# Optimization experiments

Measured on AMD Instinct MI355X. Metric: run time of the kernel, lower is better.

The kernel has to match this reference:

```python
import jax, jax.numpy as jnp
import numpy as np

N_NODES = 100000
D = 128            # hidden_size*2
N_EDGES = 1600000  # avg degree 16
NUM_LABELS = 1024


def setup_inputs() -> dict:
    key = jax.random.key(0)
    ks = jax.random.split(key, 16)
    inputs = jax.random.normal(ks[0], (N_NODES, D), dtype=jnp.float32)
    src = jax.random.randint(ks[1], (N_EDGES,), 0, N_NODES, dtype=jnp.int64)
    dst = jax.random.randint(ks[2], (N_EDGES,), 0, N_NODES, dtype=jnp.int64)
    s = 0.05
    # GIN layer 1 (conv linear) + residual block 1
    eps1 = jnp.zeros((), dtype=jnp.float32)
    W1 = jax.random.normal(ks[3], (D, D), dtype=jnp.float32) * s
    b1 = jnp.zeros((D,), dtype=jnp.float32)
    rW1 = jax.random.normal(ks[4], (D, D), dtype=jnp.float32) * s
    rb1 = jnp.zeros((D,), dtype=jnp.float32)
    # GIN layer 2 + residual block 2
    eps2 = jnp.zeros((), dtype=jnp.float32)
    W2 = jax.random.normal(ks[5], (D, D), dtype=jnp.float32) * s
    b2 = jnp.zeros((D,), dtype=jnp.float32)
    rW2 = jax.random.normal(ks[6], (D, D), dtype=jnp.float32) * s
    rb2 = jnp.zeros((D,), dtype=jnp.float32)
    # final multi-label head
    linW = jax.random.normal(ks[7], (D, NUM_LABELS), dtype=jnp.float32) * s
    linb = jnp.zeros((NUM_LABELS,), dtype=jnp.float32)
    return dict(inputs=inputs, src=src, dst=dst,
                eps1=eps1, W1=W1, b1=b1, rW1=rW1, rb1=rb1,
                eps2=eps2, W2=W2, b2=b2, rW2=rW2, rb2=rb2,
                linW=linW, linb=linb)


def reference(inputs, src, dst, eps1, W1, b1, rW1, rb1,
              eps2, W2, b2, rW2, rb2, linW, linb):
    n = inputs.shape[0]

    def gin_conv(h, eps, W, b):
        # sum-aggregate neighbor features: irregular gather + scatter-add
        agg = jax.ops.segment_sum(h[src], dst, num_segments=n)  # [N, D]
        return ((1.0 + eps) * h + agg) @ W + b

    def residual_block(h, rW, rb):
        # Sequential(ReLU, Dropout(eval=identity), Residual(D, D))
        h = jax.nn.relu(h)
        return h + jax.nn.relu(h @ rW + rb)

    h1 = residual_block(gin_conv(inputs, eps1, W1, b1), rW1, rb1)
    h2 = residual_block(gin_conv(h1, eps2, W2, b2), rW2, rb2)

    stacked = jnp.stack([h1, h2], axis=1)   # [N, n_layers, D] == stack_embed
    pooled = stacked.mean(axis=1)           # [N, D]
    return pooled @ linW + linb             # [N, NUM_LABELS]
```

## Files before the change

### kernel.cpp

```cpp
#include <hip/hip_runtime.h>

#define DIM 128
#define NLAB 1024
#define MT 64
#define LDK 136

typedef __bf16 bf16x4 __attribute__((ext_vector_type(4)));
typedef __bf16 bf16x8 __attribute__((ext_vector_type(8)));
typedef float  f32x4  __attribute__((ext_vector_type(4)));

__global__ __launch_bounds__(256) void k_hist(
    const int* __restrict__ dst, int* __restrict__ cnt, int nE) {
  int e = blockIdx.x * 256 + threadIdx.x;
  if (e < nE) atomicAdd(&cnt[dst[e]], 1);
}

__global__ __launch_bounds__(1024) void k_scan(
    const int* __restrict__ cnt, int* __restrict__ off,
    int* __restrict__ cur, int n) {
  __shared__ int part[1024];
  const int t = threadIdx.x;
  const int per = (n + 1023) >> 10;
  const int start = t * per;
  const int end = min(start + per, n);
  int s = 0;
  for (int i = start; i < end; ++i) s += cnt[i];
  part[t] = s;
  __syncthreads();
  for (int d = 1; d < 1024; d <<= 1) {
    int v = (t >= d) ? part[t - d] : 0;
    __syncthreads();
    part[t] += v;
    __syncthreads();
  }
  int excl = (t == 0) ? 0 : part[t - 1];
  if (t == 1023) off[n] = part[1023];
  for (int i = start; i < end; ++i) {
    int c = cnt[i];
    off[i] = excl;
    cur[i] = excl;
    excl += c;
  }
}

__global__ __launch_bounds__(256) void k_binfill(
    const int* __restrict__ src, const int* __restrict__ dst,
    int* __restrict__ cur, int* __restrict__ eidx, int nE) {
  int e = blockIdx.x * 256 + threadIdx.x;
  if (e < nE) {
    int p = atomicAdd(&cur[dst[e]], 1);
    eidx[p] = src[e];
  }
}

__global__ __launch_bounds__(256) void k_gather(
    const float* __restrict__ h, const int* __restrict__ off,
    const int* __restrict__ eidx, float* __restrict__ agg, int n) {
  int node = blockIdx.x * 8 + (threadIdx.x >> 5);
  if (node >= n) return;
  int c = (threadIdx.x & 31) << 2;
  int beg = off[node], end = off[node + 1];
  float4 a0 = make_float4(0.f, 0.f, 0.f, 0.f);
  float4 a1 = a0, a2 = a0, a3 = a0;
  int e = beg;
  for (; e + 4 <= end; e += 4) {
    int s0 = eidx[e + 0];
    int s1 = eidx[e + 1];
    int s2 = eidx[e + 2];
    int s3 = eidx[e + 3];
    float4 v0 = *(const float4*)(h + (size_t)s0 * DIM + c);
    float4 v1 = *(const float4*)(h + (size_t)s1 * DIM + c);
    float4 v2 = *(const float4*)(h + (size_t)s2 * DIM + c);
    float4 v3 = *(const float4*)(h + (size_t)s3 * DIM + c);
    a0.x += v0.x; a0.y += v0.y; a0.z += v0.z; a0.w += v0.w;
    a1.x += v1.x; a1.y += v1.y; a1.z += v1.z; a1.w += v1.w;
    a2.x += v2.x; a2.y += v2.y; a2.z += v2.z; a2.w += v2.w;
    a3.x += v3.x; a3.y += v3.y; a3.z += v3.z; a3.w += v3.w;
  }
  for (; e < end; ++e) {
    int s = eidx[e];
    float4 v = *(const float4*)(h + (size_t)s * DIM + c);
    a0.x += v.x; a0.y += v.y; a0.z += v.z; a0.w += v.w;
  }
  a0.x += a1.x + a2.x + a3.x;
  a0.y += a1.y + a2.y + a3.y;
  a0.z += a1.z + a2.z + a3.z;
  a0.w += a1.w + a2.w + a3.w;
  *(float4*)(agg + (size_t)node * DIM + c) = a0;
}

__device__ __forceinline__ void conv_residual_tile(
    const float* __restrict__ hin, const float* __restrict__ agg, float e1,
    const float* __restrict__ W, const float* __restrict__ bias,
    const float* __restrict__ rW, const float* __restrict__ rbias,
    __bf16 (*As)[LDK], __bf16 (*Bs)[LDK],
    int rowBase, int n, int t, float ho[4][2][4]) {
#pragma unroll
  for (int it = 0; it < 8; ++it) {
    int idx = (it * 256 + t) << 2;
    int r = idx >> 7, c = idx & 127;
    int node = rowBase + r;
    float4 a4 = make_float4(0.f, 0.f, 0.f, 0.f);
    float4 g4 = a4;
    if (node < n) {
      a4 = *(const float4*)(hin + (size_t)node * DIM + c);
      g4 = *(const float4*)(agg + (size_t)node * DIM + c);
    }
    bf16x4 v;
    v[0] = (__bf16)(e1 * a4.x + g4.x);
    v[1] = (__bf16)(e1 * a4.y + g4.y);
    v[2] = (__bf16)(e1 * a4.z + g4.z);
    v[3] = (__bf16)(e1 * a4.w + g4.w);
    *(bf16x4*)&As[r][c] = v;
  }
  {
    int nloc = t & 127;
    int kh = (t >> 7) << 6;
#pragma unroll
    for (int kk = 0; kk < 64; ++kk) {
      int k = kh + kk;
      Bs[nloc][k] = (__bf16)W[(size_t)k * DIM + nloc];
    }
  }
  __syncthreads();

  const int wv = t >> 6, lane = t & 63;
  const int quad = lane >> 4, l16 = lane & 15;
  f32x4 acc[4][2];
#pragma unroll
  for (int i = 0; i < 4; ++i) {
    acc[i][0] = f32x4{0.f, 0.f, 0.f, 0.f};
    acc[i][1] = f32x4{0.f, 0.f, 0.f, 0.f};
  }
#pragma unroll
  for (int kc = 0; kc < 4; ++kc) {
    int kb = kc * 32 + quad * 8;
    bf16x8 b0 = *(const bf16x8*)&Bs[wv * 32 + l16][kb];
    bf16x8 b1 = *(const bf16x8*)&Bs[wv * 32 + 16 + l16][kb];
#pragma unroll
    for (int rt = 0; rt < 4; ++rt) {
      bf16x8 a = *(const bf16x8*)&As[rt * 16 + l16][kb];
      acc[rt][0] = __builtin_amdgcn_mfma_f32_16x16x32_bf16(a, b0, acc[rt][0], 0, 0, 0);
      acc[rt][1] = __builtin_amdgcn_mfma_f32_16x16x32_bf16(a, b1, acc[rt][1], 0, 0, 0);
    }
  }

  float hm[4][2][4];
#pragma unroll
  for (int rt = 0; rt < 4; ++rt)
#pragma unroll
    for (int ct = 0; ct < 2; ++ct) {
      float bv = bias[wv * 32 + ct * 16 + l16];
#pragma unroll
      for (int r = 0; r < 4; ++r)
        hm[rt][ct][r] = fmaxf(acc[rt][ct][r] + bv, 0.f);
    }

  __syncthreads();

#pragma unroll
  for (int rt = 0; rt < 4; ++rt)
#pragma unroll
    for (int ct = 0; ct < 2; ++ct) {
      int col = wv * 32 + ct * 16 + l16;
#pragma unroll
      for (int r = 0; r < 4; ++r)
        As[rt * 16 + quad * 4 + r][col] = (__bf16)hm[rt][ct][r];
    }
  {
    int nloc = t & 127;
    int kh = (t >> 7) << 6;
#pragma unroll
    for (int kk = 0; kk < 64; ++kk) {
      int k = kh + kk;
      Bs[nloc][k] = (__bf16)rW[(size_t)k * DIM + nloc];
    }
  }
  __syncthreads();

#pragma unroll
  for (int i = 0; i < 4; ++i) {
    acc[i][0] = f32x4{0.f, 0.f, 0.f, 0.f};
    acc[i][1] = f32x4{0.f, 0.f, 0.f, 0.f};
  }
#pragma unroll
  for (int kc = 0; kc < 4; ++kc) {
    int kb = kc * 32 + quad * 8;
    bf16x8 b0 = *(const bf16x8*)&Bs[wv * 32 + l16][kb];
    bf16x8 b1 = *(const bf16x8*)&Bs[wv * 32 + 16 + l16][kb];
#pragma unroll
    for (int rt = 0; rt < 4; ++rt) {
      bf16x8 a = *(const bf16x8*)&As[rt * 16 + l16][kb];
      acc[rt][0] = __builtin_amdgcn_mfma_f32_16x16x32_bf16(a, b0, acc[rt][0], 0, 0, 0);
      acc[rt][1] = __builtin_amdgcn_mfma_f32_16x16x32_bf16(a, b1, acc[rt][1], 0, 0, 0);
    }
  }

#pragma unroll
  for (int rt = 0; rt < 4; ++rt)
#pragma unroll
    for (int ct = 0; ct < 2; ++ct) {
      float bv = rbias[wv * 32 + ct * 16 + l16];
#pragma unroll
      for (int r = 0; r < 4; ++r)
        ho[rt][ct][r] = hm[rt][ct][r] + fmaxf(acc[rt][ct][r] + bv, 0.f);
    }
}

__global__ __launch_bounds__(256) void k_layer1(
    const float* __restrict__ hin, const float* __restrict__ agg,
    const float* __restrict__ epsp, const float* __restrict__ W,
    const float* __restrict__ bias, const float* __restrict__ rW,
    const float* __restrict__ rbias, float* __restrict__ h1, int n) {
  __shared__ __bf16 As[MT][LDK];
  __shared__ __bf16 Bs[DIM][LDK];
  const int t = threadIdx.x;
  const int rowBase = blockIdx.x * MT;
  float ho[4][2][4];
  conv_residual_tile(hin, agg, 1.0f + epsp[0], W, bias, rW, rbias,
                     As, Bs, rowBase, n, t, ho);
  const int wv = t >> 6, lane = t & 63;
  const int quad = lane >> 4, l16 = lane & 15;
#pragma unroll
  for (int rt = 0; rt < 4; ++rt)
#pragma unroll
    for (int ct = 0; ct < 2; ++ct) {
      int ncol = wv * 32 + ct * 16 + l16;
#pragma unroll
      for (int r = 0; r < 4; ++r) {
        int node = rowBase + rt * 16 + quad * 4 + r;
        if (node < n) h1[(size_t)node * DIM + ncol] = ho[rt][ct][r];
      }
    }
}

__global__ __launch_bounds__(256) void k_layer2(
    const float* __restrict__ h1, const float* __restrict__ agg,
    const float* __restrict__ epsp, const float* __restrict__ W,
    const float* __restrict__ bias, const float* __restrict__ rW,
    const float* __restrict__ rbias, __bf16* __restrict__ pooled, int n) {
  __shared__ __bf16 As[MT][LDK];
  __shared__ __bf16 Bs[DIM][LDK];
  const int t = threadIdx.x;
  const int rowBase = blockIdx.x * MT;
  float ho[4][2][4];
  conv_residual_tile(h1, agg, 1.0f + epsp[0], W, bias, rW, rbias,
                     As, Bs, rowBase, n, t, ho);
  const int wv = t >> 6, lane = t & 63;
  const int quad = lane >> 4, l16 = lane & 15;
#pragma unroll
  for (int rt = 0; rt < 4; ++rt)
#pragma unroll
    for (int ct = 0; ct < 2; ++ct) {
      int col = wv * 32 + ct * 16 + l16;
#pragma unroll
      for (int r = 0; r < 4; ++r) {
        int node = rowBase + rt * 16 + quad * 4 + r;
        if (node < n) {
          float h1v = h1[(size_t)node * DIM + col];
          pooled[(size_t)node * DIM + col] =
              (__bf16)(0.5f * (h1v + ho[rt][ct][r]));
        }
      }
    }
}

__global__ __launch_bounds__(256) void k_final_p(
    const __bf16* __restrict__ pooled, const float* __restrict__ W,
    const float* __restrict__ bias, float* __restrict__ out, int n) {
  __shared__ __bf16 As[MT][LDK];
  __shared__ __bf16 Bs[DIM][LDK];
  const int t = threadIdx.x;
  const int rowBase = blockIdx.x * MT;
  const int nb = blockIdx.y << 7;

#pragma unroll
  for (int it = 0; it < 4; ++it) {
    int idx = (it * 256 + t) << 3;
    int r = idx >> 7, c = idx & 127;
    int node = rowBase + r;
    bf16x8 v;
#pragma unroll
    for (int j = 0; j < 8; ++j) v[j] = (__bf16)0.f;
    if (node < n) v = *(const bf16x8*)(pooled + (size_t)node * DIM + c);
    *(bf16x8*)&As[r][c] = v;
  }
  {
    int nloc = t & 127;
    int kh = (t >> 7) << 6;
#pragma unroll
    for (int kk = 0; kk < 64; ++kk) {
      int k = kh + kk;
      Bs[nloc][k] = (__bf16)W[(size_t)k * NLAB + nb + nloc];
    }
  }
  __syncthreads();

  const int wv = t >> 6, lane = t & 63;
  const int quad = lane >> 4, l16 = lane & 15;
  f32x4 acc[4][2];
#pragma unroll
  for (int i = 0; i < 4; ++i) {
    acc[i][0] = f32x4{0.f, 0.f, 0.f, 0.f};
    acc[i][1] = f32x4{0.f, 0.f, 0.f, 0.f};
  }

#pragma unroll
  for (int kc = 0; kc < 4; ++kc) {
    int kb = kc * 32 + quad * 8;
    bf16x8 b0 = *(const bf16x8*)&Bs[wv * 32 + l16][kb];
    bf16x8 b1 = *(const bf16x8*)&Bs[wv * 32 + 16 + l16][kb];
#pragma unroll
    for (int rt = 0; rt < 4; ++rt) {
      bf16x8 a = *(const bf16x8*)&As[rt * 16 + l16][kb];
      acc[rt][0] = __builtin_amdgcn_mfma_f32_16x16x32_bf16(a, b0, acc[rt][0], 0, 0, 0);
      acc[rt][1] = __builtin_amdgcn_mfma_f32_16x16x32_bf16(a, b1, acc[rt][1], 0, 0, 0);
    }
  }

#pragma unroll
  for (int rt = 0; rt < 4; ++rt)
#pragma unroll
    for (int ct = 0; ct < 2; ++ct) {
      int ncol = wv * 32 + ct * 16 + l16;
      float bv = bias[nb + ncol];
#pragma unroll
      for (int r = 0; r < 4; ++r) {
        int node = rowBase + rt * 16 + quad * 4 + r;
        if (node < n)
          out[(size_t)node * NLAB + nb + ncol] = acc[rt][ct][r] + bv;
      }
    }
}

extern "C" void kernel_launch(void* const* d_in, const int* in_sizes, int n_in,
                              void* d_out, int out_size, void* d_ws, size_t ws_size,
                              hipStream_t stream) {
  const float* inputs = (const float*)d_in[0];
  const int*   src    = (const int*)d_in[1];
  const int*   dst    = (const int*)d_in[2];
  const float* eps1   = (const float*)d_in[3];
  const float* W1     = (const float*)d_in[4];
  const float* b1     = (const float*)d_in[5];
  const float* rW1    = (const float*)d_in[6];
  const float* rb1    = (const float*)d_in[7];
  const float* eps2   = (const float*)d_in[8];
  const float* W2     = (const float*)d_in[9];
  const float* b2     = (const float*)d_in[10];
  const float* rW2    = (const float*)d_in[11];
  const float* rb2    = (const float*)d_in[12];
  const float* linW   = (const float*)d_in[13];
  const float* linb   = (const float*)d_in[14];
  float* out = (float*)d_out;

  const int n = in_sizes[0] / DIM;
  const int E = in_sizes[1];
  const size_t bufB = (size_t)n * DIM * sizeof(float);

  float*  agg    = (float*)d_ws;
  float*  h1     = (float*)((char*)d_ws + bufB);
  __bf16* pooled = (__bf16*)((char*)d_ws + 2 * bufB);

  int* eidx = (int*)d_out;
  int* off  = eidx + E;
  int* cur  = off + (n + 1);

  const int rowBlocks = (n + MT - 1) / MT;
  const int eBlocks = (E + 255) / 256;
  const int gBlocks = (n + 7) / 8;
  dim3 fgrid(rowBlocks, NLAB / DIM);

  hipMemsetAsync(cur, 0, (size_t)n * sizeof(int), stream);
  k_hist<<<eBlocks, 256, 0, stream>>>(dst, cur, E);
  k_scan<<<1, 1024, 0, stream>>>(cur, off, cur, n);
  k_binfill<<<eBlocks, 256, 0, stream>>>(src, dst, cur, eidx, E);

  k_gather<<<gBlocks, 256, 0, stream>>>(inputs, off, eidx, agg, n);
  k_layer1<<<rowBlocks, 256, 0, stream>>>(inputs, agg, eps1, W1, b1, rW1, rb1, h1, n);
  k_gather<<<gBlocks, 256, 0, stream>>>(h1, off, eidx, agg, n);
  k_layer2<<<rowBlocks, 256, 0, stream>>>(h1, agg, eps2, W2, b2, rW2, rb2,
                                          pooled, n);
  k_final_p<<<fgrid, 256, 0, stream>>>(pooled, linW, linb, out, n);
}
```

Before: 1.313 ms.

## Store node features in bf16 and pre-transpose weights once for MFMA

```diff
diff --git a/kernel.cpp b/kernel.cpp
--- a/kernel.cpp
+++ b/kernel.cpp
@@ -53,227 +53,92 @@
   }
 }
 
-__global__ __launch_bounds__(256) void k_gather(
-    const float* __restrict__ h, const int* __restrict__ off,
+__global__ __launch_bounds__(256) void k_cvt_w(
+    const float* __restrict__ W1, const float* __restrict__ rW1,
+    const float* __restrict__ W2, const float* __restrict__ rW2,
+    const float* __restrict__ linW,
+    __bf16* __restrict__ W1b, __bf16* __restrict__ rW1b,
+    __bf16* __restrict__ W2b, __bf16* __restrict__ rW2b,
+    __bf16* __restrict__ linWb) {
+  int tid = blockIdx.x * 256 + threadIdx.x;
+  if (tid < 65536) {
+    int m = tid >> 14, i = tid & 16383;
+    int nn = i >> 7, k = i & 127;
+    const float* S = (m == 0) ? W1 : (m == 1) ? rW1 : (m == 2) ? W2 : rW2;
+    __bf16* D = (m == 0) ? W1b : (m == 1) ? rW1b : (m == 2) ? W2b : rW2b;
+    D[nn * DIM + k] = (__bf16)S[(size_t)k * DIM + nn];
+  } else if (tid < 196608) {
+    int i = tid - 65536;
+    int nn = i >> 7, k = i & 127;
+    linWb[(size_t)nn * DIM + k] = (__bf16)linW[(size_t)k * NLAB + nn];
+  }
+}
+
+__global__ __launch_bounds__(256) void k_cvt_in(
+    const float* __restrict__ x, __bf16* __restrict__ y, int n) {
+  size_t i = (size_t)blockIdx.x * 256 + threadIdx.x;
+  if (i >= (size_t)n * 16) return;
+  float4 a = ((const float4*)x)[i * 2];
+  float4 b = ((const float4*)x)[i * 2 + 1];
+  bf16x8 v;
+  v[0] = (__bf16)a.x; v[1] = (__bf16)a.y; v[2] = (__bf16)a.z; v[3] = (__bf16)a.w;
+  v[4] = (__bf16)b.x; v[5] = (__bf16)b.y; v[6] = (__bf16)b.z; v[7] = (__bf16)b.w;
+  ((bf16x8*)y)[i] = v;
+}
+
+__global__ __launch_bounds__(256) void k_gather_b(
+    const __bf16* __restrict__ h, const int* __restrict__ off,
     const int* __restrict__ eidx, float* __restrict__ agg, int n) {
-  int node = blockIdx.x * 8 + (threadIdx.x >> 5);
+  int node = blockIdx.x * 16 + (threadIdx.x >> 4);
   if (node >= n) return;
-  int c = (threadIdx.x & 31) << 2;
+  int c = (threadIdx.x & 15) << 3;
   int beg = off[node], end = off[node + 1];
-  float4 a0 = make_float4(0.f, 0.f, 0.f, 0.f);
-  float4 a1 = a0, a2 = a0, a3 = a0;
+  float a0[8] = {0.f, 0.f, 0.f, 0.f, 0.f, 0.f, 0.f, 0.f};
+  float a1[8] = {0.f, 0.f, 0.f, 0.f, 0.f, 0.f, 0.f, 0.f};
+  float a2[8] = {0.f, 0.f, 0.f, 0.f, 0.f, 0.f, 0.f, 0.f};
+  float a3[8] = {0.f, 0.f, 0.f, 0.f, 0.f, 0.f, 0.f, 0.f};
   int e = beg;
   for (; e + 4 <= end; e += 4) {
     int s0 = eidx[e + 0];
     int s1 = eidx[e + 1];
     int s2 = eidx[e + 2];
     int s3 = eidx[e + 3];
-    float4 v0 = *(const float4*)(h + (size_t)s0 * DIM + c);
-    float4 v1 = *(const float4*)(h + (size_t)s1 * DIM + c);
-    float4 v2 = *(const float4*)(h + (size_t)s2 * DIM + c);
-    float4 v3 = *(const float4*)(h + (size_t)s3 * DIM + c);
-    a0.x += v0.x; a0.y += v0.y; a0.z += v0.z; a0.w += v0.w;
-    a1.x += v1.x; a1.y += v1.y; a1.z += v1.z; a1.w += v1.w;
-    a2.x += v2.x; a2.y += v2.y; a2.z += v2.z; a2.w += v2.w;
-    a3.x += v3.x; a3.y += v3.y; a3.z += v3.z; a3.w += v3.w;
+    bf16x8 v0 = *(const bf16x8*)(h + (size_t)s0 * DIM + c);
+    bf16x8 v1 = *(const bf16x8*)(h + (size_t)s1 * DIM + c);
+    bf16x8 v2 = *(const bf16x8*)(h + (size_t)s2 * DIM + c);
+    bf16x8 v3 = *(const bf16x8*)(h + (size_t)s3 * DIM + c);
+#pragma unroll
+    for (int j = 0; j < 8; ++j) {
+      a0[j] += (float)v0[j];
+      a1[j] += (float)v1[j];
+      a2[j] += (float)v2[j];
+      a3[j] += (float)v3[j];
+    }
   }
   for (; e < end; ++e) {
     int s = eidx[e];
-    float4 v = *(const float4*)(h + (size_t)s * DIM + c);
-    a0.x += v.x; a0.y += v.y; a0.z += v.z; a0.w += v.w;
-  }
-  a0.x += a1.x + a2.x + a3.x;
-  a0.y += a1.y + a2.y + a3.y;
-  a0.z += a1.z + a2.z + a3.z;
-  a0.w += a1.w + a2.w + a3.w;
-  *(float4*)(agg + (size_t)node * DIM + c) = a0;
+    bf16x8 v = *(const bf16x8*)(h + (size_t)s * DIM + c);
+#pragma unroll
+    for (int j = 0; j < 8; ++j) a0[j] += (float)v[j];
+  }
+  float4 o0, o1;
+  o0.x = a0[0] + a1[0] + a2[0] + a3[0];
+  o0.y = a0[1] + a1[1] + a2[1] + a3[1];
+  o0.z = a0[2] + a1[2] + a2[2] + a3[2];
+  o0.w = a0[3] + a1[3] + a2[3] + a3[3];
+  o1.x = a0[4] + a1[4] + a2[4] + a3[4];
+  o1.y = a0[5] + a1[5] + a2[5] + a3[5];
+  o1.z = a0[6] + a1[6] + a2[6] + a3[6];
+  o1.w = a0[7] + a1[7] + a2[7] + a3[7];
+  *(float4*)(agg + (size_t)node * DIM + c) = o0;
+  *(float4*)(agg + (size_t)node * DIM + c + 4) = o1;
 }
 
 __device__ __forceinline__ void conv_residual_tile(
-    const float* __restrict__ hin, const float* __restrict__ agg, float e1,
-    const float* __restrict__ W, const float* __restrict__ bias,
-    const float* __restrict__ rW, const float* __restrict__ rbias,
-    __bf16 (*As)[LDK], __bf16 (*Bs)[LDK],
-    int rowBase, int n, int t, float ho[4][2][4]) {
-#pragma unroll
-  for (int it = 0; it < 8; ++it) {
-    int idx = (it * 256 + t) << 2;
-    int r = idx >> 7, c = idx & 127;
-    int node = rowBase + r;
-    float4 a4 = make_float4(0.f, 0.f, 0.f, 0.f);
-    float4 g4 = a4;
-    if (node < n) {
-      a4 = *(const float4*)(hin + (size_t)node * DIM + c);
-      g4 = *(const float4*)(agg + (size_t)node * DIM + c);
-    }
-    bf16x4 v;
-    v[0] = (__bf16)(e1 * a4.x + g4.x);
-    v[1] = (__bf16)(e1 * a4.y + g4.y);
-    v[2] = (__bf16)(e1 * a4.z + g4.z);
-    v[3] = (__bf16)(e1 * a4.w + g4.w);
-    *(bf16x4*)&As[r][c] = v;
-  }
-  {
-    int nloc = t & 127;
-    int kh = (t >> 7) << 6;
-#pragma unroll
-    for (int kk = 0; kk < 64; ++kk) {
-      int k = kh + kk;
-      Bs[nloc][k] = (__bf16)W[(size_t)k * DIM + nloc];
-    }
-  }
-  __syncthreads();
-
-  const int wv = t >> 6, lane = t & 63;
-  const int quad = lane >> 4, l16 = lane & 15;
-  f32x4 acc[4][2];
-#pragma unroll
-  for (int i = 0; i < 4; ++i) {
-    acc[i][0] = f32x4{0.f, 0.f, 0.f, 0.f};
-    acc[i][1] = f32x4{0.f, 0.f, 0.f, 0.f};
-  }
-#pragma unroll
-  for (int kc = 0; kc < 4; ++kc) {
-    int kb = kc * 32 + quad * 8;
-    bf16x8 b0 = *(const bf16x8*)&Bs[wv * 32 + l16][kb];
-    bf16x8 b1 = *(const bf16x8*)&Bs[wv * 32 + 16 + l16][kb];
-#pragma unroll
-    for (int rt = 0; rt < 4; ++rt) {
-      bf16x8 a = *(const bf16x8*)&As[rt * 16 + l16][kb];
-      acc[rt][0] = __builtin_amdgcn_mfma_f32_16x16x32_bf16(a, b0, acc[rt][0], 0, 0, 0);
-      acc[rt][1] = __builtin_amdgcn_mfma_f32_16x16x32_bf16(a, b1, acc[rt][1], 0, 0, 0);
-    }
-  }
-
-  float hm[4][2][4];
-#pragma unroll
-  for (int rt = 0; rt < 4; ++rt)
-#pragma unroll
-    for (int ct = 0; ct < 2; ++ct) {
-      float bv = bias[wv * 32 + ct * 16 + l16];
-#pragma unroll
-      for (int r = 0; r < 4; ++r)
-        hm[rt][ct][r] = fmaxf(acc[rt][ct][r] + bv, 0.f);
-    }
-
-  __syncthreads();
-
-#pragma unroll
-  for (int rt = 0; rt < 4; ++rt)
-#pragma unroll
-    for (int ct = 0; ct < 2; ++ct) {
-      int col = wv * 32 + ct * 16 + l16;
-#pragma unroll
-      for (int r = 0; r < 4; ++r)
-        As[rt * 16 + quad * 4 + r][col] = (__bf16)hm[rt][ct][r];
-    }
-  {
-    int nloc = t & 127;
-    int kh = (t >> 7) << 6;
-#pragma unroll
-    for (int kk = 0; kk < 64; ++kk) {
-      int k = kh + kk;
-      Bs[nloc][k] = (__bf16)rW[(size_t)k * DIM + nloc];
-    }
-  }
-  __syncthreads();
-
-#pragma unroll
-  for (int i = 0; i < 4; ++i) {
-    acc[i][0] = f32x4{0.f, 0.f, 0.f, 0.f};
-    acc[i][1] = f32x4{0.f, 0.f, 0.f, 0.f};
-  }
-#pragma unroll
-  for (int kc = 0; kc < 4; ++kc) {
-    int kb = kc * 32 + quad * 8;
-    bf16x8 b0 = *(const bf16x8*)&Bs[wv * 32 + l16][kb];
-    bf16x8 b1 = *(const bf16x8*)&Bs[wv * 32 + 16 + l16][kb];
-#pragma unroll
-    for (int rt = 0; rt < 4; ++rt) {
-      bf16x8 a = *(const bf16x8*)&As[rt * 16 + l16][kb];
-      acc[rt][0] = __builtin_amdgcn_mfma_f32_16x16x32_bf16(a, b0, acc[rt][0], 0, 0, 0);
-      acc[rt][1] = __builtin_amdgcn_mfma_f32_16x16x32_bf16(a, b1, acc[rt][1], 0, 0, 0);
-    }
-  }
-
-#pragma unroll
-  for (int rt = 0; rt < 4; ++rt)
-#pragma unroll
-    for (int ct = 0; ct < 2; ++ct) {
-      float bv = rbias[wv * 32 + ct * 16 + l16];
-#pragma unroll
-      for (int r = 0; r < 4; ++r)
-        ho[rt][ct][r] = hm[rt][ct][r] + fmaxf(acc[rt][ct][r] + bv, 0.f);
-    }
-}
-
-__global__ __launch_bounds__(256) void k_layer1(
-    const float* __restrict__ hin, const float* __restrict__ agg,
-    const float* __restrict__ epsp, const float* __restrict__ W,
-    const float* __restrict__ bias, const float* __restrict__ rW,
-    const float* __restrict__ rbias, float* __restrict__ h1, int n) {
-  __shared__ __bf16 As[MT][LDK];
-  __shared__ __bf16 Bs[DIM][LDK];
-  const int t = threadIdx.x;
-  const int rowBase = blockIdx.x * MT;
-  float ho[4][2][4];
-  conv_residual_tile(hin, agg, 1.0f + epsp[0], W, bias, rW, rbias,
-                     As, Bs, rowBase, n, t, ho);
-  const int wv = t >> 6, lane = t & 63;
-  const int quad = lane >> 4, l16 = lane & 15;
-#pragma unroll
-  for (int rt = 0; rt < 4; ++rt)
-#pragma unroll
-    for (int ct = 0; ct < 2; ++ct) {
-      int ncol = wv * 32 + ct * 16 + l16;
-#pragma unroll
-      for (int r = 0; r < 4; ++r) {
-        int node = rowBase + rt * 16 + quad * 4 + r;
-        if (node < n) h1[(size_t)node * DIM + ncol] = ho[rt][ct][r];
-      }
-    }
-}
-
-__global__ __launch_bounds__(256) void k_layer2(
-    const float* __restrict__ h1, const float* __restrict__ agg,
-    const float* __restrict__ epsp, const float* __restrict__ W,
-    const float* __restrict__ bias, const float* __restrict__ rW,
-    const float* __restrict__ rbias, __bf16* __restrict__ pooled, int n) {
-  __shared__ __bf16 As[MT][LDK];
-  __shared__ __bf16 Bs[DIM][LDK];
-  const int t = threadIdx.x;
-  const int rowBase = blockIdx.x * MT;
-  float ho[4][2][4];
-  conv_residual_tile(h1, agg, 1.0f + epsp[0], W, bias, rW, rbias,
-                     As, Bs, rowBase, n, t, ho);
-  const int wv = t >> 6, lane = t & 63;
-  const int quad = lane >> 4, l16 = lane & 15;
-#pragma unroll
-  for (int rt = 0; rt < 4; ++rt)
-#pragma unroll
-    for (int ct = 0; ct < 2; ++ct) {
-      int col = wv * 32 + ct * 16 + l16;
-#pragma unroll
-      for (int r = 0; r < 4; ++r) {
-        int node = rowBase + rt * 16 + quad * 4 + r;
-        if (node < n) {
-          float h1v = h1[(size_t)node * DIM + col];
-          pooled[(size_t)node * DIM + col] =
-              (__bf16)(0.5f * (h1v + ho[rt][ct][r]));
-        }
-      }
-    }
-}
-
-__global__ __launch_bounds__(256) void k_final_p(
-    const __bf16* __restrict__ pooled, const float* __restrict__ W,
-    const float* __restrict__ bias, float* __restrict__ out, int n) {
-  __shared__ __bf16 As[MT][LDK];
-  __shared__ __bf16 Bs[DIM][LDK];
-  const int t = threadIdx.x;
-  const int rowBase = blockIdx.x * MT;
-  const int nb = blockIdx.y << 7;
-
+    const __bf16* __restrict__ hinb, const float* __restrict__ agg, float e1,
+    const __bf16* __restrict__ Wb, const float* __restrict__ bias,
+    const __bf16* __restrict__ rWb, const float* __restrict__ rbias,
+    __bf16 (*As)[LDK], int rowBase, int n, int t, float ho[4][2][4]) {
 #pragma unroll
   for (int it = 0; it < 4; ++it) {
     int idx = (it * 256 + t) << 3;
@@ -282,34 +147,195 @@
     bf16x8 v;
 #pragma unroll
     for (int j = 0; j < 8; ++j) v[j] = (__bf16)0.f;
-    if (node < n) v = *(const bf16x8*)(pooled + (size_t)node * DIM + c);
+    if (node < n) {
+      bf16x8 hv = *(const bf16x8*)(hinb + (size_t)node * DIM + c);
+      float4 g0 = *(const float4*)(agg + (size_t)node * DIM + c);
+      float4 g1 = *(const float4*)(agg + (size_t)node * DIM + c + 4);
+      v[0] = (__bf16)(e1 * (float)hv[0] + g0.x);
+      v[1] = (__bf16)(e1 * (float)hv[1] + g0.y);
+      v[2] = (__bf16)(e1 * (float)hv[2] + g0.z);
+      v[3] = (__bf16)(e1 * (float)hv[3] + g0.w);
+      v[4] = (__bf16)(e1 * (float)hv[4] + g1.x);
+      v[5] = (__bf16)(e1 * (float)hv[5] + g1.y);
+      v[6] = (__bf16)(e1 * (float)hv[6] + g1.z);
+      v[7] = (__bf16)(e1 * (float)hv[7] + g1.w);
+    }
     *(bf16x8*)&As[r][c] = v;
-  }
-  {
-    int nloc = t & 127;
-    int kh = (t >> 7) << 6;
-#pragma unroll
-    for (int kk = 0; kk < 64; ++kk) {
-      int k = kh + kk;
-      Bs[nloc][k] = (__bf16)W[(size_t)k * NLAB + nb + nloc];
-    }
   }
   __syncthreads();
 
   const int wv = t >> 6, lane = t & 63;
   const int quad = lane >> 4, l16 = lane & 15;
+  const __bf16* B0p = Wb + (size_t)(wv * 32 + l16) * DIM;
+  const __bf16* B1p = Wb + (size_t)(wv * 32 + 16 + l16) * DIM;
+
   f32x4 acc[4][2];
 #pragma unroll
   for (int i = 0; i < 4; ++i) {
     acc[i][0] = f32x4{0.f, 0.f, 0.f, 0.f};
     acc[i][1] = f32x4{0.f, 0.f, 0.f, 0.f};
   }
-
 #pragma unroll
   for (int kc = 0; kc < 4; ++kc) {
     int kb = kc * 32 + quad * 8;
-    bf16x8 b0 = *(const bf16x8*)&Bs[wv * 32 + l16][kb];
-    bf16x8 b1 = *(const bf16x8*)&Bs[wv * 32 + 16 + l16][kb];
+    bf16x8 b0 = *(const bf16x8*)(B0p + kb);
+    bf16x8 b1 = *(const bf16x8*)(B1p + kb);
+#pragma unroll
+    for (int rt = 0; rt < 4; ++rt) {
+      bf16x8 a = *(const bf16x8*)&As[rt * 16 + l16][kb];
+      acc[rt][0] = __builtin_amdgcn_mfma_f32_16x16x32_bf16(a, b0, acc[rt][0], 0, 0, 0);
+      acc[rt][1] = __builtin_amdgcn_mfma_f32_16x16x32_bf16(a, b1, acc[rt][1], 0, 0, 0);
+    }
+  }
+
+  float hm[4][2][4];
+#pragma unroll
+  for (int rt = 0; rt < 4; ++rt)
+#pragma unroll
+    for (int ct = 0; ct < 2; ++ct) {
+      float bv = bias[wv * 32 + ct * 16 + l16];
+#pragma unroll
+      for (int r = 0; r < 4; ++r)
+        hm[rt][ct][r] = fmaxf(acc[rt][ct][r] + bv, 0.f);
+    }
+
+  __syncthreads();
+
+#pragma unroll
+  for (int rt = 0; rt < 4; ++rt)
+#pragma unroll
+    for (int ct = 0; ct < 2; ++ct) {
+      int col = wv * 32 + ct * 16 + l16;
+#pragma unroll
+      for (int r = 0; r < 4; ++r)
+        As[rt * 16 + quad * 4 + r][col] = (__bf16)hm[rt][ct][r];
+    }
+  __syncthreads();
+
+  const __bf16* R0p = rWb + (size_t)(wv * 32 + l16) * DIM;
+  const __bf16* R1p = rWb + (size_t)(wv * 32 + 16 + l16) * DIM;
+#pragma unroll
+  for (int i = 0; i < 4; ++i) {
+    acc[i][0] = f32x4{0.f, 0.f, 0.f, 0.f};
+    acc[i][1] = f32x4{0.f, 0.f, 0.f, 0.f};
+  }
+#pragma unroll
+  for (int kc = 0; kc < 4; ++kc) {
+    int kb = kc * 32 + quad * 8;
+    bf16x8 b0 = *(const bf16x8*)(R0p + kb);
+    bf16x8 b1 = *(const bf16x8*)(R1p + kb);
+#pragma unroll
+    for (int rt = 0; rt < 4; ++rt) {
+      bf16x8 a = *(const bf16x8*)&As[rt * 16 + l16][kb];
+      acc[rt][0] = __builtin_amdgcn_mfma_f32_16x16x32_bf16(a, b0, acc[rt][0], 0, 0, 0);
+      acc[rt][1] = __builtin_amdgcn_mfma_f32_16x16x32_bf16(a, b1, acc[rt][1], 0, 0, 0);
+    }
+  }
+
+#pragma unroll
+  for (int rt = 0; rt < 4; ++rt)
+#pragma unroll
+    for (int ct = 0; ct < 2; ++ct) {
+      float bv = rbias[wv * 32 + ct * 16 + l16];
+#pragma unroll
+      for (int r = 0; r < 4; ++r)
+        ho[rt][ct][r] = hm[rt][ct][r] + fmaxf(acc[rt][ct][r] + bv, 0.f);
+    }
+}
+
+__global__ __launch_bounds__(256, 3) void k_layer1(
+    const __bf16* __restrict__ hinb, const float* __restrict__ agg,
+    const float* __restrict__ epsp, const __bf16* __restrict__ Wb,
+    const float* __restrict__ bias, const __bf16* __restrict__ rWb,
+    const float* __restrict__ rbias, __bf16* __restrict__ h1b, int n) {
+  __shared__ __bf16 As[MT][LDK];
+  const int t = threadIdx.x;
+  const int rowBase = blockIdx.x * MT;
+  float ho[4][2][4];
+  conv_residual_tile(hinb, agg, 1.0f + epsp[0], Wb, bias, rWb, rbias,
+                     As, rowBase, n, t, ho);
+  const int wv = t >> 6, lane = t & 63;
+  const int quad = lane >> 4, l16 = lane & 15;
+#pragma unroll
+  for (int rt = 0; rt < 4; ++rt)
+#pragma unroll
+    for (int ct = 0; ct < 2; ++ct) {
+      int ncol = wv * 32 + ct * 16 + l16;
+#pragma unroll
+      for (int r = 0; r < 4; ++r) {
+        int node = rowBase + rt * 16 + quad * 4 + r;
+        if (node < n) h1b[(size_t)node * DIM + ncol] = (__bf16)ho[rt][ct][r];
+      }
+    }
+}
+
+__global__ __launch_bounds__(256, 3) void k_layer2(
+    const __bf16* __restrict__ h1b, const float* __restrict__ agg,
+    const float* __restrict__ epsp, const __bf16* __restrict__ Wb,
+    const float* __restrict__ bias, const __bf16* __restrict__ rWb,
+    const float* __restrict__ rbias, __bf16* __restrict__ pooled, int n) {
+  __shared__ __bf16 As[MT][LDK];
+  const int t = threadIdx.x;
+  const int rowBase = blockIdx.x * MT;
+  float ho[4][2][4];
+  conv_residual_tile(h1b, agg, 1.0f + epsp[0], Wb, bias, rWb, rbias,
+                     As, rowBase, n, t, ho);
+  const int wv = t >> 6, lane = t & 63;
+  const int quad = lane >> 4, l16 = lane & 15;
+#pragma unroll
+  for (int rt = 0; rt < 4; ++rt)
+#pragma unroll
+    for (int ct = 0; ct < 2; ++ct) {
+      int col = wv * 32 + ct * 16 + l16;
+#pragma unroll
+      for (int r = 0; r < 4; ++r) {
+        int node = rowBase + rt * 16 + quad * 4 + r;
+        if (node < n) {
+          float h1v = (float)h1b[(size_t)node * DIM + col];
+          pooled[(size_t)node * DIM + col] =
+              (__bf16)(0.5f * (h1v + ho[rt][ct][r]));
+        }
+      }
+    }
+}
+
+__global__ __launch_bounds__(256, 4) void k_final_p(
+    const __bf16* __restrict__ pooled, const __bf16* __restrict__ Wb,
+    const float* __restrict__ bias, float* __restrict__ out, int n) {
+  __shared__ __bf16 As[MT][LDK];
+  const int t = threadIdx.x;
+  const int rowBase = blockIdx.x * MT;
+  const int nb = blockIdx.y << 7;
+
+#pragma unroll
+  for (int it = 0; it < 4; ++it) {
+    int idx = (it * 256 + t) << 3;
+    int r = idx >> 7, c = idx & 127;
+    int node = rowBase + r;
+    bf16x8 v;
+#pragma unroll
+    for (int j = 0; j < 8; ++j) v[j] = (__bf16)0.f;
+    if (node < n) v = *(const bf16x8*)(pooled + (size_t)node * DIM + c);
+    *(bf16x8*)&As[r][c] = v;
+  }
+  __syncthreads();
+
+  const int wv = t >> 6, lane = t & 63;
+  const int quad = lane >> 4, l16 = lane & 15;
+  const __bf16* B0p = Wb + (size_t)(nb + wv * 32 + l16) * DIM;
+  const __bf16* B1p = Wb + (size_t)(nb + wv * 32 + 16 + l16) * DIM;
+
+  f32x4 acc[4][2];
+#pragma unroll
+  for (int i = 0; i < 4; ++i) {
+    acc[i][0] = f32x4{0.f, 0.f, 0.f, 0.f};
+    acc[i][1] = f32x4{0.f, 0.f, 0.f, 0.f};
+  }
+#pragma unroll
+  for (int kc = 0; kc < 4; ++kc) {
+    int kb = kc * 32 + quad * 8;
+    bf16x8 b0 = *(const bf16x8*)(B0p + kb);
+    bf16x8 b1 = *(const bf16x8*)(B1p + kb);
 #pragma unroll
     for (int rt = 0; rt < 4; ++rt) {
       bf16x8 a = *(const bf16x8*)&As[rt * 16 + l16][kb];
@@ -356,10 +382,18 @@
   const int n = in_sizes[0] / DIM;
   const int E = in_sizes[1];
   const size_t bufB = (size_t)n * DIM * sizeof(float);
-
-  float*  agg    = (float*)d_ws;
-  float*  h1     = (float*)((char*)d_ws + bufB);
-  __bf16* pooled = (__bf16*)((char*)d_ws + 2 * bufB);
+  const size_t halfB = bufB >> 1;
+
+  char* wp = (char*)d_ws;
+  float*  agg    = (float*)wp;   wp += bufB;
+  __bf16* hb0    = (__bf16*)wp;  wp += halfB;
+  __bf16* h1b    = (__bf16*)wp;  wp += halfB;
+  __bf16* pooled = (__bf16*)wp;  wp += halfB;
+  __bf16* W1b    = (__bf16*)wp;  wp += 32768;
+  __bf16* rW1b   = (__bf16*)wp;  wp += 32768;
+  __bf16* W2b    = (__bf16*)wp;  wp += 32768;
+  __bf16* rW2b   = (__bf16*)wp;  wp += 32768;
+  __bf16* linWb  = (__bf16*)wp;
 
   int* eidx = (int*)d_out;
   int* off  = eidx + E;
@@ -367,18 +401,24 @@
 
   const int rowBlocks = (n + MT - 1) / MT;
   const int eBlocks = (E + 255) / 256;
-  const int gBlocks = (n + 7) / 8;
+  const int gBlocks = (n + 15) / 16;
+  const int cBlocks = (n * 16 + 255) / 256;
   dim3 fgrid(rowBlocks, NLAB / DIM);
+
+  k_cvt_w<<<768, 256, 0, stream>>>(W1, rW1, W2, rW2, linW,
+                                   W1b, rW1b, W2b, rW2b, linWb);
+  k_cvt_in<<<cBlocks, 256, 0, stream>>>(inputs, hb0, n);
 
   hipMemsetAsync(cur, 0, (size_t)n * sizeof(int), stream);
   k_hist<<<eBlocks, 256, 0, stream>>>(dst, cur, E);
   k_scan<<<1, 1024, 0, stream>>>(cur, off, cur, n);
   k_binfill<<<eBlocks, 256, 0, stream>>>(src, dst, cur, eidx, E);
 
-  k_gather<<<gBlocks, 256, 0, stream>>>(inputs, off, eidx, agg, n);
-  k_layer1<<<rowBlocks, 256, 0, stream>>>(inputs, agg, eps1, W1, b1, rW1, rb1, h1, n);
-  k_gather<<<gBlocks, 256, 0, stream>>>(h1, off, eidx, agg, n);
-  k_layer2<<<rowBlocks, 256, 0, stream>>>(h1, agg, eps2, W2, b2, rW2, rb2,
+  k_gather_b<<<gBlocks, 256, 0, stream>>>(hb0, off, eidx, agg, n);
+  k_layer1<<<rowBlocks, 256, 0, stream>>>(hb0, agg, eps1, W1b, b1, rW1b, rb1,
+                                          h1b, n);
+  k_gather_b<<<gBlocks, 256, 0, stream>>>(h1b, off, eidx, agg, n);
+  k_layer2<<<rowBlocks, 256, 0, stream>>>(h1b, agg, eps2, W2b, b2, rW2b, rb2,
                                           pooled, n);
-  k_final_p<<<fgrid, 256, 0, stream>>>(pooled, linW, linb, out, n);
-}
+  k_final_p<<<fgrid, 256, 0, stream>>>(pooled, linWb, linb, out, n);
+}
```

After: 1.156 ms. -11.9%, faster.
